# Performance work log

Measured on AMD Instinct MI355X. Metric: run time of the kernel, lower is better.

## Reference

```python
import jax, jax.numpy as jnp
import numpy as np

D_MODEL = 1024
N_HEADS = 16
D_HEAD = D_MODEL // N_HEADS
B, T = 4, 2048


def setup_inputs() -> dict:
    key = jax.random.key(0)
    ks = jax.random.split(key, 7)
    s = 0.02
    q = jax.random.normal(ks[0], (B, T, D_MODEL), dtype=jnp.float32)
    k = jax.random.normal(ks[1], (B, T, D_MODEL), dtype=jnp.float32)
    v = jax.random.normal(ks[2], (B, T, D_MODEL), dtype=jnp.float32)
    # causal mask, True = masked (strict upper triangle)
    mask = jnp.triu(jnp.ones((T, T), dtype=bool), k=1)[None, None, :, :]
    Wq = jax.random.normal(ks[3], (D_MODEL, D_MODEL), dtype=jnp.float32) * s
    Wk = jax.random.normal(ks[4], (D_MODEL, D_MODEL), dtype=jnp.float32) * s
    Wv = jax.random.normal(ks[5], (D_MODEL, D_MODEL), dtype=jnp.float32) * s
    Wo = jax.random.normal(ks[6], (D_MODEL, D_MODEL), dtype=jnp.float32) * s
    return {"q": q, "k": k, "v": v, "mask": mask,
            "Wq": Wq, "Wk": Wk, "Wv": Wv, "Wo": Wo}


def reference(q, k, v, mask, Wq, Wk, Wv, Wo):
    H, Dh = N_HEADS, D_HEAD
    scale = Dh ** -0.5

    def split(t):  # [B,T,D] -> [B,H,T,Dh]
        Bt, Tt, _ = t.shape
        return t.reshape(Bt, Tt, H, Dh).transpose(0, 2, 1, 3)

    # torch Linear (no bias): y = x @ W.T
    Q = split(q @ Wq.T)
    K = split(k @ Wk.T)
    V = split(v @ Wv.T)

    scores = jnp.einsum('bhqd,bhkd->bhqk', Q, K) * scale
    scores = jnp.where(mask, -jnp.inf, scores)
    attn = jax.nn.softmax(scores, axis=-1)
    attn = jnp.nan_to_num(attn)  # fully-masked rows -> 0
    out = jnp.einsum('bhqk,bhkd->bhqd', attn, V)
    out = out.transpose(0, 2, 1, 3).reshape(q.shape[0], q.shape[1], H * Dh)
    return out @ Wo.T
```

## Files before the change

### kernel.cpp

```cpp
#include <hip/hip_runtime.h>
#include <stdint.h>

#define D_MODEL 1024
#define N_HEADS 16
#define D_HEAD 64
#define BATCH 4
#define SEQ 2048
#define MTOT (BATCH * SEQ)

typedef unsigned short u16;
typedef __attribute__((ext_vector_type(8))) short bf16x8;
typedef __attribute__((ext_vector_type(4))) float f32x4;

#define MFMA(a, b, c) __builtin_amdgcn_mfma_f32_16x16x32_bf16((a), (b), (c), 0, 0, 0)
#define LOG2E 1.4426950408889634f
#define SC (0.125f * LOG2E)

static __device__ __forceinline__ u16 f2bf(float f) {
  unsigned u = __builtin_bit_cast(unsigned, f);
  u += 0x7fffu + ((u >> 16) & 1u);
  return (u16)(u >> 16);
}
static __device__ __forceinline__ u16 f2bf_t(float f) {
  return (u16)(__builtin_bit_cast(unsigned, f) >> 16);
}

static __device__ __forceinline__ void gload_lds16(const void* g, void* l) {
  __builtin_amdgcn_global_load_lds(
      (const __attribute__((address_space(1))) void*)g,
      (__attribute__((address_space(3))) void*)l, 16, 0, 0);
}

__global__ __launch_bounds__(256) void cvt3(const float* __restrict__ a,
                                            const float* __restrict__ b,
                                            const float* __restrict__ c,
                                            u16* __restrict__ oa, u16* __restrict__ ob,
                                            u16* __restrict__ oc) {
  const int z = blockIdx.y;
  const float* in = (z == 0) ? a : (z == 1) ? b : c;
  u16* out = (z == 0) ? oa : (z == 1) ? ob : oc;
  int i = blockIdx.x * 256 + threadIdx.x;
  float4 v = ((const float4*)in)[i];
  ushort4 o;
  o.x = f2bf(v.x); o.y = f2bf(v.y); o.z = f2bf(v.z); o.w = f2bf(v.w);
  ((ushort4*)out)[i] = o;
}

__global__ __launch_bounds__(256) void cvt4(const float* __restrict__ a,
                                            const float* __restrict__ b,
                                            const float* __restrict__ c,
                                            const float* __restrict__ d,
                                            u16* __restrict__ oa, u16* __restrict__ ob,
                                            u16* __restrict__ oc, u16* __restrict__ od) {
  const int z = blockIdx.y;
  const float* in = (z == 0) ? a : (z == 1) ? b : (z == 2) ? c : d;
  u16* out = (z == 0) ? oa : (z == 1) ? ob : (z == 2) ? oc : od;
  const float s = (z == 0) ? SC : 1.0f;
  int i = blockIdx.x * 256 + threadIdx.x;
  float4 v = ((const float4*)in)[i];
  ushort4 o;
  o.x = f2bf(v.x * s); o.y = f2bf(v.y * s); o.z = f2bf(v.z * s); o.w = f2bf(v.w * s);
  ((ushort4*)out)[i] = o;
}

#define BM 256
#define BN 128
#define BK 64
#define NKT (D_MODEL / BK)

static __device__ __forceinline__ void gemm_core(const u16* __restrict__ A,
                                                 const u16* __restrict__ B,
                                                 u16* As, u16* Bs,
                                                 int m0, int n0, f32x4 acc[4][4]) {
  const int t = threadIdx.x;
  const int lane = t & 63, wave = t >> 6;
  const int wm = wave >> 1, wn = wave & 1;
  const int lrow = lane & 15, quad = lane >> 4;
  const int srow = t >> 3;
  const int swcol = (((t & 7) ^ (srow & 7)) << 3);
  const int sdst = srow * 64 + (t & 7) * 8;
  const int rsw = lrow & 7;

#pragma unroll
  for (int i = 0; i < 4; i++)
#pragma unroll
    for (int j = 0; j < 4; j++) acc[i][j] = (f32x4){0.f, 0.f, 0.f, 0.f};

#define STAGE_(kt_, bi_)                                                        \
  do {                                                                          \
    const int k0_ = (kt_)*BK;                                                   \
    u16* as_ = As + (bi_) * (BM * BK);                                          \
    u16* bs_ = Bs + (bi_) * (BN * BK);                                          \
    _Pragma("unroll") for (int r_ = 0; r_ < 4; ++r_)                            \
        gload_lds16(A + (size_t)(m0 + r_ * 64 + srow) * 1024 + k0_ + swcol,     \
                    as_ + r_ * 64 * 64 + sdst);                                 \
    _Pragma("unroll") for (int r_ = 0; r_ < 2; ++r_)                            \
        gload_lds16(B + (size_t)(n0 + r_ * 64 + srow) * 1024 + k0_ + swcol,     \
                    bs_ + r_ * 64 * 64 + sdst);                                 \
  } while (0)

  STAGE_(0, 0);
  STAGE_(1, 1);

  for (int kt = 0; kt < NKT; ++kt) {
    if (kt < NKT - 1) asm volatile("s_waitcnt vmcnt(6)" ::: "memory");
    else              asm volatile("s_waitcnt vmcnt(0)" ::: "memory");
    __builtin_amdgcn_s_barrier();
    asm volatile("" ::: "memory");

    const u16* as = As + (kt & 1) * (BM * BK);
    const u16* bs = Bs + (kt & 1) * (BN * BK);

#pragma unroll
    for (int ks = 0; ks < 2; ++ks) {
      const int cx = ((ks * 4 + quad) ^ rsw) << 3;
      bf16x8 a[4], b[4];
#pragma unroll
      for (int i = 0; i < 4; i++)
        a[i] = *(const bf16x8*)(as + (wm * 64 + i * 16 + lrow) * 64 + cx);
#pragma unroll
      for (int j = 0; j < 4; j++)
        b[j] = *(const bf16x8*)(bs + (wn * 64 + j * 16 + lrow) * 64 + cx);
      __builtin_amdgcn_s_setprio(1);
#pragma unroll
      for (int i = 0; i < 4; i++)
#pragma unroll
        for (int j = 0; j < 4; j++) acc[i][j] = MFMA(a[i], b[j], acc[i][j]);
      __builtin_amdgcn_s_setprio(0);
    }

    if (kt + 2 < NKT) {
      asm volatile("" ::: "memory");
      __builtin_amdgcn_sched_barrier(0);
      __builtin_amdgcn_s_barrier();
      STAGE_(kt + 2, kt & 1);
    }
  }
#undef STAGE_
}

__global__ __launch_bounds__(512, 2) void gemm_qkv(const u16* __restrict__ xq,
                                                   const u16* __restrict__ xk,
                                                   const u16* __restrict__ xv,
                                                   const u16* __restrict__ Wqb,
                                                   const u16* __restrict__ Wkb,
                                                   const u16* __restrict__ Wvb,
                                                   u16* __restrict__ Qb, u16* __restrict__ Kb,
                                                   u16* __restrict__ Vtg, int zbase) {
  __shared__ u16 As[2 * BM * BK];
  __shared__ u16 Bs[2 * BN * BK];
  const int z = blockIdx.z + zbase;
  const u16* A = (z == 0) ? xq : (z == 1) ? xk : xv;
  const u16* B = (z == 0) ? Wqb : (z == 1) ? Wkb : Wvb;
  const int m0 = blockIdx.x * BM, n0 = blockIdx.y * BN;

  f32x4 acc[4][4];
  gemm_core(A, B, As, Bs, m0, n0, acc);

  const int lane = threadIdx.x & 63, wave = threadIdx.x >> 6;
  const int wm = wave >> 1, wn = wave & 1;
  const int lrow = lane & 15, quad = lane >> 4;

  if (z == 2) {
    const int b = m0 >> 11;
    const int t0 = (m0 & 2047);
#pragma unroll
    for (int i = 0; i < 4; i++) {
      const int trow = t0 + wm * 64 + i * 16 + quad * 4;
#pragma unroll
      for (int j = 0; j < 4; j++) {
        const int n = n0 + wn * 64 + j * 16 + lrow;
        ushort4 pk;
        pk.x = f2bf(acc[i][j][0]); pk.y = f2bf(acc[i][j][1]);
        pk.z = f2bf(acc[i][j][2]); pk.w = f2bf(acc[i][j][3]);
        *(ushort4*)(Vtg + (size_t)b * D_MODEL * SEQ + (size_t)n * SEQ + trow) = pk;
      }
    }
  } else {
    u16* C = z ? Kb : Qb;
#pragma unroll
    for (int i = 0; i < 4; i++) {
      const int mr = m0 + wm * 64 + i * 16 + quad * 4;
#pragma unroll
      for (int j = 0; j < 4; j++) {
        const int n = n0 + wn * 64 + j * 16 + lrow;
#pragma unroll
        for (int r = 0; r < 4; r++) C[(size_t)(mr + r) * 1024 + n] = f2bf(acc[i][j][r]);
      }
    }
  }
}

__global__ __launch_bounds__(512, 2) void gemm_o(const u16* __restrict__ A,
                                                 const u16* __restrict__ B,
                                                 float* __restrict__ C) {
  __shared__ u16 As[2 * BM * BK];
  __shared__ u16 Bs[2 * BN * BK];
  const int m0 = blockIdx.x * BM, n0 = blockIdx.y * BN;

  f32x4 acc[4][4];
  gemm_core(A, B, As, Bs, m0, n0, acc);

  const int lane = threadIdx.x & 63, wave = threadIdx.x >> 6;
  const int wm = wave >> 1, wn = wave & 1;
  const int lrow = lane & 15, quad = lane >> 4;
#pragma unroll
  for (int i = 0; i < 4; i++) {
    const int mr = m0 + wm * 64 + i * 16 + quad * 4;
#pragma unroll
    for (int j = 0; j < 4; j++) {
      const int n = n0 + wn * 64 + j * 16 + lrow;
#pragma unroll
      for (int r = 0; r < 4; r++) C[(size_t)(mr + r) * 1024 + n] = acc[i][j][r];
    }
  }
}

__global__ __launch_bounds__(256) void attn_causal(const u16* __restrict__ Qb,
                                                   const u16* __restrict__ Kb,
                                                   const u16* __restrict__ Vtg,
                                                   u16* __restrict__ Ob) {
  __shared__ u16 QPs[128 * 64];
  __shared__ u16 Ks[64 * 64];
  __shared__ u16 Vs[64 * 64];

  const int t = threadIdx.x;
  const int lane = t & 63, wave = t >> 6;
  const int lrow = lane & 15, quad = lane >> 4;
  const int wb = wave * 32;
  const int bh = blockIdx.x;
  const int b = bh >> 4, h = bh & 15;
  const int col0 = h * 64;
  const size_t rowbase = (size_t)b * SEQ;
  const size_t vbase = (size_t)b * (size_t)D_MODEL * SEQ;
  const int srow = t >> 3;
  const int swcol = (((t & 7) ^ (srow & 7)) << 3);
  const int pchunk = (t & 7) * 8;
  const int rsw = lrow & 7;

  bf16x8 bOnes;
  {
    const short ov = (lrow == 0) ? (short)0x3F80 : (short)0;
#pragma unroll
    for (int e = 0; e < 8; ++e) bOnes[e] = ov;
  }

  for (int part = 0; part < 2; ++part) {
    const int qt = part ? (15 - (int)blockIdx.y) : (int)blockIdx.y;
    const int qrow0 = qt * 128;

#pragma unroll
    for (int r = 0; r < 4; ++r) {
      int rr = r * 32 + srow;
      gload_lds16(Qb + (rowbase + qrow0 + rr) * D_MODEL + col0 + swcol,
                  QPs + rr * 64 + pchunk);
    }

    bf16x8 bQ[2][2];
    f32x4 oacc[2][4];
    f32x4 lacc[2];
#pragma unroll
    for (int mf = 0; mf < 2; mf++) {
#pragma unroll
      for (int df = 0; df < 4; df++) oacc[mf][df] = (f32x4){0.f, 0.f, 0.f, 0.f};
      lacc[mf] = (f32x4){0.f, 0.f, 0.f, 0.f};
    }

    const int nkt = 2 * qt + 2;
    for (int kt = 0; kt < nkt; ++kt) {
      const int j0 = kt * 64;
      __syncthreads();
#pragma unroll
      for (int r = 0; r < 2; ++r) {
        int rr = r * 32 + srow;
        gload_lds16(Kb + (rowbase + j0 + rr) * D_MODEL + col0 + swcol,
                    Ks + rr * 64 + pchunk);
        gload_lds16(Vtg + vbase + (size_t)(col0 + rr) * SEQ + j0 + swcol,
                    Vs + rr * 64 + pchunk);
      }
      __syncthreads();

      if (kt == 0) {
#pragma unroll
        for (int mf = 0; mf < 2; ++mf)
#pragma unroll
          for (int ks = 0; ks < 2; ++ks)
            bQ[mf][ks] = *(const bf16x8*)(QPs + (wb + mf * 16 + lrow) * 64 +
                                          (((ks * 4 + quad) ^ rsw) << 3));
      }

      const bool diag = (kt >= 2 * qt);
#pragma unroll
      for (int mf = 0; mf < 2; ++mf) {
        f32x4 st[4];
#pragma unroll
        for (int jf = 0; jf < 4; jf++) st[jf] = (f32x4){0.f, 0.f, 0.f, 0.f};
#pragma unroll
        for (int ks = 0; ks < 2; ++ks) {
          const int cx = ((ks * 4 + quad) ^ rsw) << 3;
#pragma unroll
          for (int jf = 0; jf < 4; jf++) {
            bf16x8 aK = *(const bf16x8*)(Ks + (jf * 16 + lrow) * 64 + cx);
            st[jf] = MFMA(aK, bQ[mf][ks], st[jf]);
          }
        }
        const int m = wb + mf * 16 + lrow;
        const int gm = qrow0 + m;
#pragma unroll
        for (int jf = 0; jf < 4; jf++) {
          ushort4 pk;
#pragma unroll
          for (int r = 0; r < 4; r++) {
            float p = __builtin_amdgcn_exp2f(st[jf][r]);
            const int gj = j0 + jf * 16 + quad * 4 + r;
            if (diag && gj > gm) p = 0.f;
            ((u16*)&pk)[r] = f2bf_t(p);
          }
          const int j = jf * 16 + quad * 4;
          *(ushort4*)(QPs + m * 64 + ((((j >> 3) ^ (m & 7)) << 3) | (j & 7))) = pk;
        }
      }

#pragma unroll
      for (int ks = 0; ks < 2; ++ks) {
        const int cx = ((ks * 4 + quad) ^ rsw) << 3;
        bf16x8 aP[2];
#pragma unroll
        for (int mf = 0; mf < 2; ++mf)
          aP[mf] = *(const bf16x8*)(QPs + (wb + mf * 16 + lrow) * 64 + cx);
        lacc[0] = MFMA(aP[0], bOnes, lacc[0]);
        lacc[1] = MFMA(aP[1], bOnes, lacc[1]);
#pragma unroll
        for (int df = 0; df < 4; df++) {
          bf16x8 bV = *(const bf16x8*)(Vs + (df * 16 + lrow) * 64 + cx);
          oacc[0][df] = MFMA(aP[0], bV, oacc[0][df]);
          oacc[1][df] = MFMA(aP[1], bV, oacc[1][df]);
        }
      }
    }
    __syncthreads();

    float linv[2][4];
#pragma unroll
    for (int mf = 0; mf < 2; mf++)
#pragma unroll
      for (int r = 0; r < 4; r++)
        linv[mf][r] = 1.0f / __shfl(lacc[mf][r], lane & 48);

#pragma unroll
    for (int mf = 0; mf < 2; mf++)
#pragma unroll
      for (int r = 0; r < 4; r++) {
        u16* orow = Ob + (rowbase + qrow0 + wb + mf * 16 + quad * 4 + r) * D_MODEL + col0;
#pragma unroll
        for (int df = 0; df < 4; df++)
          orow[df * 16 + lrow] = f2bf(oacc[mf][df][r] * linv[mf][r]);
      }
  }
}

extern "C" void kernel_launch(void* const* d_in, const int* in_sizes, int n_in,
                              void* d_out, int out_size, void* d_ws, size_t ws_size,
                              hipStream_t stream) {
  const float* q  = (const float*)d_in[0];
  const float* k  = (const float*)d_in[1];
  const float* v  = (const float*)d_in[2];
  const float* Wq = (const float*)d_in[4];
  const float* Wk = (const float*)d_in[5];
  const float* Wv = (const float*)d_in[6];
  const float* Wo = (const float*)d_in[7];
  float* out = (float*)d_out;

  char* ws = (char*)d_ws;
  const size_t MB = 1 << 20;
  u16* xq  = (u16*)(ws);
  u16* xk  = (u16*)(ws + 16 * MB);
  u16* xv  = (u16*)(ws + 32 * MB);
  u16* Wqb = (u16*)(ws + 48 * MB);
  u16* Wkb = (u16*)(ws + 50 * MB);
  u16* Wvb = (u16*)(ws + 52 * MB);
  u16* Wob = (u16*)(ws + 54 * MB);
  u16* Qb  = (u16*)(ws + 56 * MB);

  const dim3 cb(256);
  const dim3 gb(512);
  cvt3<<<dim3(MTOT * D_MODEL / 4 / 256, 3), cb, 0, stream>>>(q, k, v, xq, xk, xv);
  cvt4<<<dim3(D_MODEL * D_MODEL / 4 / 256, 4), cb, 0, stream>>>(Wq, Wk, Wv, Wo,
                                                                Wqb, Wkb, Wvb, Wob);

  if (ws_size >= 104 * MB) {
    u16* Kb  = (u16*)(ws + 72 * MB);
    u16* Vtg = (u16*)(ws + 88 * MB);
    gemm_qkv<<<dim3(32, 8, 3), gb, 0, stream>>>(xq, xk, xv, Wqb, Wkb, Wvb,
                                                Qb, Kb, Vtg, 0);
    attn_causal<<<dim3(64, 8), cb, 0, stream>>>(Qb, Kb, Vtg, xq);
    gemm_o<<<dim3(32, 8), gb, 0, stream>>>(xq, Wob, out);
  } else {
    u16* Kb  = (u16*)(ws);
    u16* Vtg = (u16*)(ws + 16 * MB);
    u16* Oatt = (u16*)(ws + 32 * MB);
    gemm_qkv<<<dim3(32, 8, 1), gb, 0, stream>>>(xq, xq, xq, Wqb, Wqb, Wqb,
                                                Qb, Qb, Qb, 0);
    gemm_qkv<<<dim3(32, 8, 1), gb, 0, stream>>>(xk, xk, xk, Wkb, Wkb, Wkb,
                                                Kb, Kb, Kb, 1);
    gemm_qkv<<<dim3(32, 8, 1), gb, 0, stream>>>(xv, xv, xv, Wvb, Wvb, Wvb,
                                                Vtg, Vtg, Vtg, 2);
    attn_causal<<<dim3(64, 8), cb, 0, stream>>>(Qb, Kb, Vtg, Oatt);
    gemm_o<<<dim3(32, 8), gb, 0, stream>>>(Oatt, Wob, out);
  }
}
```

Baseline: 320.1 us.

## Triple-buffer LDS in GEMM and attention with prefetch issued two tiles ahead

Both GEMM kernels move from two shared-memory buffers to three. The prefetch of tile kt+2 is now issued right after the top-of-loop barrier, which drops the second barrier per iteration. The causal attention kernel previously loaded each K/V tile synchronously between two __syncthreads. It now gets a three-deep K/V ring with vmcnt-based waits, so global loads overlap the QK, softmax and PV MFMA work. The cost is more LDS per block (about 64KB for attention, about 147KB for the GEMMs), which may lower occupancy, plus more register pressure from holding both k-substeps of fragments.

```diff
diff --git a/kernel.cpp b/kernel.cpp
--- a/kernel.cpp
+++ b/kernel.cpp
@@ -67,6 +67,8 @@
 #define BN 128
 #define BK 64
 #define NKT (D_MODEL / BK)
+#define ASZ (BM * BK)
+#define BSZ (BN * BK)
 
 static __device__ __forceinline__ void gemm_core(const u16* __restrict__ A,
                                                  const u16* __restrict__ B,
@@ -89,8 +91,8 @@
 #define STAGE_(kt_, bi_)                                                        \
   do {                                                                          \
     const int k0_ = (kt_)*BK;                                                   \
-    u16* as_ = As + (bi_) * (BM * BK);                                          \
-    u16* bs_ = Bs + (bi_) * (BN * BK);                                          \
+    u16* as_ = As + (bi_)*ASZ;                                                  \
+    u16* bs_ = Bs + (bi_)*BSZ;                                                  \
     _Pragma("unroll") for (int r_ = 0; r_ < 4; ++r_)                            \
         gload_lds16(A + (size_t)(m0 + r_ * 64 + srow) * 1024 + k0_ + swcol,     \
                     as_ + r_ * 64 * 64 + sdst);                                 \
@@ -108,33 +110,32 @@
     __builtin_amdgcn_s_barrier();
     asm volatile("" ::: "memory");
 
-    const u16* as = As + (kt & 1) * (BM * BK);
-    const u16* bs = Bs + (kt & 1) * (BN * BK);
-
+    if (kt + 2 < NKT) STAGE_(kt + 2, (kt + 2) % 3);
+
+    const u16* as = As + (kt % 3) * ASZ;
+    const u16* bs = Bs + (kt % 3) * BSZ;
+
+    bf16x8 a[2][4], b[2][4];
 #pragma unroll
     for (int ks = 0; ks < 2; ++ks) {
       const int cx = ((ks * 4 + quad) ^ rsw) << 3;
-      bf16x8 a[4], b[4];
 #pragma unroll
       for (int i = 0; i < 4; i++)
-        a[i] = *(const bf16x8*)(as + (wm * 64 + i * 16 + lrow) * 64 + cx);
+        a[ks][i] = *(const bf16x8*)(as + (wm * 64 + i * 16 + lrow) * 64 + cx);
 #pragma unroll
       for (int j = 0; j < 4; j++)
-        b[j] = *(const bf16x8*)(bs + (wn * 64 + j * 16 + lrow) * 64 + cx);
+        b[ks][j] = *(const bf16x8*)(bs + (wn * 64 + j * 16 + lrow) * 64 + cx);
+    }
+#pragma unroll
+    for (int ks = 0; ks < 2; ++ks) {
       __builtin_amdgcn_s_setprio(1);
 #pragma unroll
       for (int i = 0; i < 4; i++)
 #pragma unroll
-        for (int j = 0; j < 4; j++) acc[i][j] = MFMA(a[i], b[j], acc[i][j]);
+        for (int j = 0; j < 4; j++) acc[i][j] = MFMA(a[ks][i], b[ks][j], acc[i][j]);
       __builtin_amdgcn_s_setprio(0);
     }
-
-    if (kt + 2 < NKT) {
-      asm volatile("" ::: "memory");
-      __builtin_amdgcn_sched_barrier(0);
-      __builtin_amdgcn_s_barrier();
-      STAGE_(kt + 2, kt & 1);
-    }
+    __builtin_amdgcn_sched_barrier(0);
   }
 #undef STAGE_
 }
@@ -147,8 +148,8 @@
                                                    const u16* __restrict__ Wvb,
                                                    u16* __restrict__ Qb, u16* __restrict__ Kb,
                                                    u16* __restrict__ Vtg, int zbase) {
-  __shared__ u16 As[2 * BM * BK];
-  __shared__ u16 Bs[2 * BN * BK];
+  __shared__ u16 As[3 * ASZ];
+  __shared__ u16 Bs[3 * BSZ];
   const int z = blockIdx.z + zbase;
   const u16* A = (z == 0) ? xq : (z == 1) ? xk : xv;
   const u16* B = (z == 0) ? Wqb : (z == 1) ? Wkb : Wvb;
@@ -194,8 +195,8 @@
 __global__ __launch_bounds__(512, 2) void gemm_o(const u16* __restrict__ A,
                                                  const u16* __restrict__ B,
                                                  float* __restrict__ C) {
-  __shared__ u16 As[2 * BM * BK];
-  __shared__ u16 Bs[2 * BN * BK];
+  __shared__ u16 As[3 * ASZ];
+  __shared__ u16 Bs[3 * BSZ];
   const int m0 = blockIdx.x * BM, n0 = blockIdx.y * BN;
 
   f32x4 acc[4][4];
@@ -221,8 +222,8 @@
                                                    const u16* __restrict__ Vtg,
                                                    u16* __restrict__ Ob) {
   __shared__ u16 QPs[128 * 64];
-  __shared__ u16 Ks[64 * 64];
-  __shared__ u16 Vs[64 * 64];
+  __shared__ u16 Ks[3 * 64 * 64];
+  __shared__ u16 Vs[3 * 64 * 64];
 
   const int t = threadIdx.x;
   const int lane = t & 63, wave = t >> 6;
@@ -238,6 +239,20 @@
   const int pchunk = (t & 7) * 8;
   const int rsw = lrow & 7;
 
+#define KVSTAGE_(kt_, bi_)                                                      \
+  do {                                                                          \
+    const int j0_ = (kt_)*64;                                                   \
+    u16* ks_ = Ks + (bi_)*4096;                                                 \
+    u16* vs_ = Vs + (bi_)*4096;                                                 \
+    _Pragma("unroll") for (int r_ = 0; r_ < 2; ++r_) {                          \
+      int rr_ = r_ * 32 + srow;                                                 \
+      gload_lds16(Kb + (rowbase + j0_ + rr_) * D_MODEL + col0 + swcol,          \
+                  ks_ + rr_ * 64 + pchunk);                                     \
+      gload_lds16(Vtg + vbase + (size_t)(col0 + rr_) * SEQ + j0_ + swcol,       \
+                  vs_ + rr_ * 64 + pchunk);                                     \
+    }                                                                           \
+  } while (0)
+
   bf16x8 bOnes;
   {
     const short ov = (lrow == 0) ? (short)0x3F80 : (short)0;
@@ -248,6 +263,7 @@
   for (int part = 0; part < 2; ++part) {
     const int qt = part ? (15 - (int)blockIdx.y) : (int)blockIdx.y;
     const int qrow0 = qt * 128;
+    const int nkt = 2 * qt + 2;
 
 #pragma unroll
     for (int r = 0; r < 4; ++r) {
@@ -255,6 +271,8 @@
       gload_lds16(Qb + (rowbase + qrow0 + rr) * D_MODEL + col0 + swcol,
                   QPs + rr * 64 + pchunk);
     }
+    KVSTAGE_(0, 0);
+    KVSTAGE_(1, 1);
 
     bf16x8 bQ[2][2];
     f32x4 oacc[2][4];
@@ -266,19 +284,16 @@
       lacc[mf] = (f32x4){0.f, 0.f, 0.f, 0.f};
     }
 
-    const int nkt = 2 * qt + 2;
     for (int kt = 0; kt < nkt; ++kt) {
-      const int j0 = kt * 64;
-      __syncthreads();
-#pragma unroll
-      for (int r = 0; r < 2; ++r) {
-        int rr = r * 32 + srow;
-        gload_lds16(Kb + (rowbase + j0 + rr) * D_MODEL + col0 + swcol,
-                    Ks + rr * 64 + pchunk);
-        gload_lds16(Vtg + vbase + (size_t)(col0 + rr) * SEQ + j0 + swcol,
-                    Vs + rr * 64 + pchunk);
-      }
-      __syncthreads();
+      if (kt < nkt - 1) asm volatile("s_waitcnt vmcnt(4)" ::: "memory");
+      else              asm volatile("s_waitcnt vmcnt(0)" ::: "memory");
+      __builtin_amdgcn_s_barrier();
+      asm volatile("" ::: "memory");
+
+      if (kt + 2 < nkt) KVSTAGE_(kt + 2, (kt + 2) % 3);
+
+      const u16* ksb = Ks + (kt % 3) * 4096;
+      const u16* vsb = Vs + (kt % 3) * 4096;
 
       if (kt == 0) {
 #pragma unroll
@@ -289,6 +304,7 @@
                                           (((ks * 4 + quad) ^ rsw) << 3));
       }
 
+      const int j0 = kt * 64;
       const bool diag = (kt >= 2 * qt);
 #pragma unroll
       for (int mf = 0; mf < 2; ++mf) {
@@ -300,7 +316,7 @@
           const int cx = ((ks * 4 + quad) ^ rsw) << 3;
 #pragma unroll
           for (int jf = 0; jf < 4; jf++) {
-            bf16x8 aK = *(const bf16x8*)(Ks + (jf * 16 + lrow) * 64 + cx);
+            bf16x8 aK = *(const bf16x8*)(ksb + (jf * 16 + lrow) * 64 + cx);
             st[jf] = MFMA(aK, bQ[mf][ks], st[jf]);
           }
         }
@@ -332,11 +348,12 @@
         lacc[1] = MFMA(aP[1], bOnes, lacc[1]);
 #pragma unroll
         for (int df = 0; df < 4; df++) {
-          bf16x8 bV = *(const bf16x8*)(Vs + (df * 16 + lrow) * 64 + cx);
+          bf16x8 bV = *(const bf16x8*)(vsb + (df * 16 + lrow) * 64 + cx);
           oacc[0][df] = MFMA(aP[0], bV, oacc[0][df]);
           oacc[1][df] = MFMA(aP[1], bV, oacc[1][df]);
         }
       }
+      __builtin_amdgcn_sched_barrier(0);
     }
     __syncthreads();
 
@@ -357,6 +374,7 @@
           orow[df * 16 + lrow] = f2bf(oacc[mf][df][r] * linv[mf][r]);
       }
   }
+#undef KVSTAGE_
 }
 
 extern "C" void kernel_launch(void* const* d_in, const int* in_sizes, int n_in,
```

New measurement: 319.2 us. No clear change (-0.3%).
